# Kernel optimization log

Hardware: AMD Instinct MI355X
Metric: run time of the kernel (lower is better)

## Reference

```python
import jax, jax.numpy as jnp
from jax import lax
import numpy as np

B, H, W = 2048, 28, 28
LATENT_EACH = 64
LATENT = 2 * LATENT_EACH  # 128
MEM_SIZE = 8192
TOPK = 10
EPS = 1e-12


def _conv(x, w, b):
    # x: NCHW, w: OIHW, 3x3 conv, padding=1 (SAME)
    y = lax.conv_general_dilated(x, w, (1, 1), 'SAME',
                                 dimension_numbers=('NCHW', 'OIHW', 'NCHW'))
    return y + b[None, :, None, None]


def _deconv(x, w, b):
    # ConvTranspose2d(k=4, stride=2, padding=1) -> out = 2*in (SAME transpose)
    # w: HWIO = (4,4,in,out)
    y = lax.conv_transpose(x, w, (2, 2), 'SAME',
                           dimension_numbers=('NCHW', 'HWIO', 'NCHW'))
    return y + b[None, :, None, None]


def _encoder(x, w1, b1, w2, b2, fcw, fcb):
    h = jax.nn.relu(_conv(x, w1, b1))
    h = jax.nn.relu(_conv(h, w2, b2))
    feat = h.mean(axis=(2, 3))  # AdaptiveAvgPool2d((1,1)) + flatten -> [B,64]
    return feat @ fcw.T + fcb


def _memory_match(z, mem):
    mn = mem / jnp.maximum(jnp.linalg.norm(mem, axis=1, keepdims=True), EPS)
    zn = z / jnp.maximum(jnp.linalg.norm(z, axis=1, keepdims=True), EPS)
    sim = zn @ mn.T                      # [B, MEM_SIZE]
    topv, topi = lax.top_k(sim, TOPK)    # [B, K]
    wts = jax.nn.softmax(topv, axis=1)   # [B, K]
    sel = mem[topi]                      # gather: [B, K, LATENT]
    return jnp.einsum('bk,bkd->bd', wts, sel)


def setup_inputs() -> dict:
    key = jax.random.key(0)
    ks = jax.random.split(key, 24)
    g = lambda k, s, scale=0.05: jax.random.normal(k, s, jnp.float32) * scale
    inp = {
        'x': jax.random.normal(ks[0], (B, 1, H, W), jnp.float32),
        # center encoder
        'ce_w1': g(ks[1], (32, 1, 3, 3)), 'ce_b1': jnp.zeros((32,), jnp.float32),
        'ce_w2': g(ks[2], (64, 32, 3, 3)), 'ce_b2': jnp.zeros((64,), jnp.float32),
        'ce_fcw': g(ks[3], (LATENT_EACH, 64)), 'ce_fcb': jnp.zeros((LATENT_EACH,), jnp.float32),
        # global encoder
        'ge_w1': g(ks[4], (32, 1, 3, 3)), 'ge_b1': jnp.zeros((32,), jnp.float32),
        'ge_w2': g(ks[5], (64, 32, 3, 3)), 'ge_b2': jnp.zeros((64,), jnp.float32),
        'ge_fcw': g(ks[6], (LATENT_EACH, 64)), 'ge_fcb': jnp.zeros((LATENT_EACH,), jnp.float32),
        # memory bank (Parameter ~ randn)
        'mem': jax.random.normal(ks[7], (MEM_SIZE, LATENT), jnp.float32),
        # decoder
        'dec_fcw': g(ks[8], (64 * 7 * 7, LATENT)), 'dec_fcb': jnp.zeros((64 * 7 * 7,), jnp.float32),
        'd_w1': g(ks[9], (4, 4, 64, 32)), 'd_b1': jnp.zeros((32,), jnp.float32),   # deconv 64->32
        'd_w2': g(ks[10], (16, 32, 3, 3)), 'd_b2': jnp.zeros((16,), jnp.float32),  # conv 32->16
        'd_w3': g(ks[11], (4, 4, 16, 8)), 'd_b3': jnp.zeros((8,), jnp.float32),    # deconv 16->8
        'd_w4': g(ks[12], (1, 8, 3, 3)), 'd_b4': jnp.zeros((1,), jnp.float32),     # conv 8->1
    }
    return inp


def reference(x, ce_w1, ce_b1, ce_w2, ce_b2, ce_fcw, ce_fcb,
              ge_w1, ge_b1, ge_w2, ge_b2, ge_fcw, ge_fcb,
              mem, dec_fcw, dec_fcb,
              d_w1, d_b1, d_w2, d_b2, d_w3, d_b3, d_w4, d_b4):
    # crop_center(x, 14): start = (28-14)//2 = 7
    x_center = x[:, :, 7:21, 7:21]
    z_center = _encoder(x_center, ce_w1, ce_b1, ce_w2, ce_b2, ce_fcw, ce_fcb)
    z_global = _encoder(x, ge_w1, ge_b1, ge_w2, ge_b2, ge_fcw, ge_fcb)
    z = jnp.concatenate([z_center, z_global], axis=1)  # [B, 128]
    z_match = _memory_match(z, mem)                    # [B, 128]
    d = (z_match @ dec_fcw.T + dec_fcb).reshape(B, 64, 7, 7)
    d = jax.nn.relu(_deconv(d, d_w1, d_b1))   # [B,32,14,14]
    d = jax.nn.relu(_conv(d, d_w2, d_b2))     # [B,16,14,14]
    d = jax.nn.relu(_deconv(d, d_w3, d_b3))   # [B,8,28,28]
    x_hat = _conv(d, d_w4, d_b4)              # [B,1,28,28]
    return x_hat
```

## Files before the change

### kernel.cpp

```cpp
#include <hip/hip_runtime.h>
#include <cfloat>
#include <cmath>

#define TPB 256

typedef _Float16 half8 __attribute__((ext_vector_type(8)));
typedef float floatx16 __attribute__((ext_vector_type(16)));
typedef float floatx4 __attribute__((ext_vector_type(4)));

__device__ __forceinline__ float wave_reduce_sum(float v) {
#pragma unroll
  for (int off = 32; off > 0; off >>= 1) v += __shfl_xor(v, off, 64);
  return v;
}

__global__ __launch_bounds__(64) void prep_bfrags(
    const float* __restrict__ ce_w2, const float* __restrict__ ge_w2,
    float* __restrict__ frags) {
  const int blk = blockIdx.x;
  const int enc = blk / 72;
  const int frag = blk % 72;
  const int ks = frag >> 2, part = (frag >> 1) & 1, nt = frag & 1;
  const int tap = ks >> 1, half = ks & 1;
  const int lane = threadIdx.x;
  const float* w2 = enc ? ge_w2 : ce_w2;
  const int n = nt * 32 + (lane & 31);
  const int cb = half * 16 + (lane >> 5) * 8;
  half8 out;
#pragma unroll
  for (int j = 0; j < 8; ++j) {
    float v = w2[(n * 32 + cb + j) * 9 + tap];
    _Float16 h = (_Float16)v;
    out[j] = (part == 0) ? h : (_Float16)((v - (float)h) * 4096.f);
  }
  *(half8*)((char*)frags + ((size_t)blk * 64 + lane) * 16) = out;
}

__global__ __launch_bounds__(64) void prep_dec1(
    const float* __restrict__ w1, float* __restrict__ frags) {
  const int blk = blockIdx.x;
  const int phase = blk >> 4, ks = blk & 15;
  const int pa = phase >> 1, pb = phase & 1;
  const int st = ks >> 2, kk = ks & 3;
  const int s = st >> 1, tt = st & 1;
  const int lane = threadIdx.x;
  const int kg = lane >> 5, n = lane & 31;
  const int tap = (pa + 2 * s) * 4 + (pb + 2 * tt);
  half8 o;
#pragma unroll
  for (int j = 0; j < 8; ++j) {
    int c = kk * 16 + kg * 8 + j;
    o[j] = (_Float16)w1[tap * 2048 + c * 32 + n];
  }
  *(half8*)((char*)frags + ((size_t)blk * 64 + lane) * 16) = o;
}

__global__ __launch_bounds__(64) void prep_dfc(
    const float* __restrict__ dfcw, float* __restrict__ frags) {
  const int blk = blockIdx.x;
  const int nt = blk >> 3, ks = blk & 7;
  const int lane = threadIdx.x;
  const int n = lane & 31, kg = lane >> 5;
  const int j = nt * 32 + n;
  const int px = j >> 6, c = j & 63;
  half8 o;
#pragma unroll
  for (int u = 0; u < 8; ++u)
    o[u] = (_Float16)dfcw[(size_t)(c * 49 + px) * 128 + ks * 16 + kg * 8 + u];
  *(half8*)((char*)frags + ((size_t)blk * 64 + lane) * 16) = o;
}

__global__ __launch_bounds__(256) void norm_kernel(
    const float* __restrict__ memg, float* __restrict__ invn) {
  const int wv = threadIdx.x >> 6, lane = threadIdx.x & 63;
  const int row = blockIdx.x * 4 + wv;
  const float* r = memg + (size_t)row * 128;
  float a = r[lane], b = r[lane + 64];
  float s = wave_reduce_sum(a * a + b * b);
  if (lane == 0) invn[row] = 1.f / fmaxf(sqrtf(s), 1e-12f);
}

template <int S, bool CENTER>
__device__ __forceinline__ void encoder_body(
    char* smem, const float* __restrict__ x, const float* __restrict__ w1,
    const float* __restrict__ b1, const float* __restrict__ b2,
    const float* __restrict__ fcw, const float* __restrict__ fcb,
    const float* __restrict__ bfrag, float* __restrict__ zout, int zoff,
    int b) {
  constexpr int SP = S + 2;
  constexpr int NBANDS = (S == 28) ? 3 : 2;
  constexpr int RMAX = 12;
  constexpr int NPIX = RMAX * SP;
  constexpr int GSTB = NPIX * 16;
  constexpr int PSTB = 4 * GSTB;

  char* h1s = smem;
  float* xs = (float*)(smem + 2 * PSTB);
  float* w1s = xs + SP * SP;
  float(*featp)[64] = (float(*)[64])(w1s + 288);

  const int t = threadIdx.x;
  const int lane = t & 63;
  const int wv = t >> 6;

  for (int e = t; e < SP * SP; e += TPB) xs[e] = 0.f;
  for (int e = t; e < 288; e += TPB) w1s[e] = w1[e];
  __syncthreads();
  const float* xb = x + (size_t)b * 784 + (CENTER ? (7 * 28 + 7) : 0);
  for (int e = t; e < S * S; e += TPB) {
    int i = e / S, j = e - i * S;
    xs[(i + 1) * SP + (j + 1)] = xb[i * 28 + j];
  }

  float sp0 = 0.f, sp1 = 0.f;
  const float bias0 = b2[lane & 31];
  const float bias1 = b2[32 + (lane & 31)];
  const int gOff = (lane >> 5) * GSTB;
  const char* bgbase = (const char*)bfrag + lane * 16;

#pragma unroll
  for (int band = 0; band < NBANDS; ++band) {
    const int BH_ = (S == 28) ? ((band < 2) ? 10 : 8) : ((band == 0) ? 10 : 4);
    const int b0 = band * 10;
    const int LIMIT = BH_ * S;
    const int MTB = (LIMIT + 31) / 32;
    const int NBLK2 = (MTB + 1) / 2;

    __syncthreads();
    for (int e = t; e < 4 * NPIX; e += TPB) {
      int g = e / NPIX;
      int pix = e - g * NPIX;
      int lr = pix / SP;
      int cw = pix - lr * SP;
      int gr = b0 - 1 + lr;
      int ebase = g * GSTB + pix * 16;
      half8 hi8 = {}, lo8 = {};
      if (gr >= 0 && gr < S && cw >= 1 && cw <= S) {
        float xv[9];
#pragma unroll
        for (int di = 0; di < 3; ++di)
#pragma unroll
          for (int dj = 0; dj < 3; ++dj)
            xv[di * 3 + dj] = xs[(gr + di) * SP + (cw - 1 + dj)];
#pragma unroll
        for (int u = 0; u < 8; ++u) {
          int ch = g * 8 + u;
          float a = b1[ch];
#pragma unroll
          for (int v = 0; v < 9; ++v) a += xv[v] * w1s[ch * 9 + v];
          a = fmaxf(a, 0.f);
          _Float16 h = (_Float16)a;
          hi8[u] = h;
          lo8[u] = (_Float16)((a - (float)h) * 4096.f);
        }
      }
      *(half8*)(h1s + ebase) = hi8;
      *(half8*)(h1s + PSTB + ebase) = lo8;
    }
    __syncthreads();
    for (int mblk = wv; mblk < NBLK2; mblk += 4) {
      const int Mt0 = mblk * 2;
      floatx16 acc[2][2][2] = {};
      int pixB[2];
#pragma unroll
      for (int im = 0; im < 2; ++im) {
        int px = (Mt0 + im) * 32 + (lane & 31);
        px = px < LIMIT ? px : LIMIT - 1;
        int r = px / S;
        int cc = px - r * S;
        pixB[im] = (r * SP + cc) * 16;
      }
#pragma unroll 3
      for (int tap = 0; tap < 9; ++tap) {
        const int di = tap / 3, dj = tap - di * 3;
        const int offT = (di * SP + dj) * 16;
#pragma unroll
        for (int half = 0; half < 2; ++half) {
          const int ks = tap * 2 + half;
          const char* bp = bgbase + ks * 4096;
          const int offA = offT + gOff + half * (2 * GSTB);
          half8 ah0 = *(const half8*)(h1s + pixB[0] + offA);
          half8 al0 = *(const half8*)(h1s + PSTB + pixB[0] + offA);
          half8 ah1 = *(const half8*)(h1s + pixB[1] + offA);
          half8 al1 = *(const half8*)(h1s + PSTB + pixB[1] + offA);
          {
            half8 bh = *(const half8*)(bp);
            half8 bl = *(const half8*)(bp + 2048);
            acc[0][0][0] = __builtin_amdgcn_mfma_f32_32x32x16_f16(
                ah0, bh, acc[0][0][0], 0, 0, 0);
            acc[0][0][1] = __builtin_amdgcn_mfma_f32_32x32x16_f16(
                ah0, bl, acc[0][0][1], 0, 0, 0);
            acc[0][0][1] = __builtin_amdgcn_mfma_f32_32x32x16_f16(
                al0, bh, acc[0][0][1], 0, 0, 0);
            acc[1][0][0] = __builtin_amdgcn_mfma_f32_32x32x16_f16(
                ah1, bh, acc[1][0][0], 0, 0, 0);
            acc[1][0][1] = __builtin_amdgcn_mfma_f32_32x32x16_f16(
                ah1, bl, acc[1][0][1], 0, 0, 0);
            acc[1][0][1] = __builtin_amdgcn_mfma_f32_32x32x16_f16(
                al1, bh, acc[1][0][1], 0, 0, 0);
          }
          {
            half8 bh = *(const half8*)(bp + 1024);
            half8 bl = *(const half8*)(bp + 3072);
            acc[0][1][0] = __builtin_amdgcn_mfma_f32_32x32x16_f16(
                ah0, bh, acc[0][1][0], 0, 0, 0);
            acc[0][1][1] = __builtin_amdgcn_mfma_f32_32x32x16_f16(
                ah0, bl, acc[0][1][1], 0, 0, 0);
            acc[0][1][1] = __builtin_amdgcn_mfma_f32_32x32x16_f16(
                al0, bh, acc[0][1][1], 0, 0, 0);
            acc[1][1][0] = __builtin_amdgcn_mfma_f32_32x32x16_f16(
                ah1, bh, acc[1][1][0], 0, 0, 0);
            acc[1][1][1] = __builtin_amdgcn_mfma_f32_32x32x16_f16(
                ah1, bl, acc[1][1][1], 0, 0, 0);
            acc[1][1][1] = __builtin_amdgcn_mfma_f32_32x32x16_f16(
                al1, bh, acc[1][1][1], 0, 0, 0);
          }
        }
      }
#pragma unroll
      for (int im = 0; im < 2; ++im)
#pragma unroll
        for (int reg = 0; reg < 16; ++reg) {
          int row = (reg & 3) + 8 * (reg >> 2) + 4 * (lane >> 5);
          int p = (Mt0 + im) * 32 + row;
          if (p < LIMIT) {
            float v0 =
                acc[im][0][0][reg] + acc[im][0][1][reg] * (1.f / 4096.f) + bias0;
            float v1 =
                acc[im][1][0][reg] + acc[im][1][1][reg] * (1.f / 4096.f) + bias1;
            sp0 += fmaxf(v0, 0.f);
            sp1 += fmaxf(v1, 0.f);
          }
        }
    }
  }
  sp0 += __shfl_xor(sp0, 32);
  sp1 += __shfl_xor(sp1, 32);
  if (lane < 32) {
    featp[wv][lane] = sp0;
    featp[wv][32 + lane] = sp1;
  }
  __syncthreads();
  if (t < 64)
    featp[0][t] = (featp[0][t] + featp[1][t] + featp[2][t] + featp[3][t]) *
                  (1.f / (S * S));
  __syncthreads();
  if (t < 64) {
    float s = 0.f;
#pragma unroll
    for (int i = 0; i < 64; ++i) s += featp[0][i] * fcw[t * 64 + i];
    zout[(size_t)b * 128 + zoff + t] = s + fcb[t];
  }
}

__global__ __launch_bounds__(256, 3) void encoders_fused(
    const float* __restrict__ x, const float* __restrict__ ce_w1,
    const float* __restrict__ ce_b1, const float* __restrict__ ce_b2,
    const float* __restrict__ ce_fcw, const float* __restrict__ ce_fcb,
    const float* __restrict__ ge_w1, const float* __restrict__ ge_b1,
    const float* __restrict__ ge_b2, const float* __restrict__ ge_fcw,
    const float* __restrict__ ge_fcb, const float* __restrict__ frags,
    float* __restrict__ z) {
  __shared__ __align__(16) char smem[51856];
  if (blockIdx.x < 2048)
    encoder_body<28, false>(smem, x, ge_w1, ge_b1, ge_b2, ge_fcw, ge_fcb,
                            frags + 18432, z, 64, blockIdx.x);
  else
    encoder_body<14, true>(smem, x, ce_w1, ce_b1, ce_b2, ce_fcw, ce_fcb, frags,
                           z, 0, blockIdx.x - 2048);
}

__global__ __launch_bounds__(256) void match_part(
    const float* __restrict__ z, const float* __restrict__ memg,
    const float* __restrict__ invn, float* __restrict__ topvw,
    int* __restrict__ topiw) {
  __shared__ __align__(16) float zs[8][128];
  __shared__ float qv[8][512];
  __shared__ int qi[8][512];
  __shared__ int qn[8];
  __shared__ float rowmin[8];

  const int t = threadIdx.x;
  const int rowbase = blockIdx.x * 8;
  const int mbase = blockIdx.y * 2048;

  for (int e = t; e < 8 * 128; e += TPB) {
    int r = e >> 7, j = e & 127;
    zs[r][j] = z[(size_t)(rowbase + r) * 128 + j];
  }
  if (t < 8) { qn[t] = 0; rowmin[t] = -FLT_MAX; }
  __syncthreads();
  {
    int wv = t >> 6, lane = t & 63;
#pragma unroll
    for (int h = 0; h < 2; ++h) {
      int r = wv + h * 4;
      float a = zs[r][lane], b = zs[r][lane + 64];
      float s = wave_reduce_sum(a * a + b * b);
      float inv = 1.f / fmaxf(sqrtf(s), 1e-12f);
      zs[r][lane] = a * inv;
      zs[r][lane + 64] = b * inv;
    }
  }
  __syncthreads();

  float av[10];
  int ai[10];
#pragma unroll
  for (int i = 0; i < 10; ++i) { av[i] = -FLT_MAX; ai[i] = 0; }

  for (int mt = 0; mt < 4; ++mt) {
    int m0 = mbase + mt * 512 + t;
    float acc0[8] = {}, acc1[8] = {};
    const float4* mr0 = (const float4*)(memg + (size_t)m0 * 128);
    const float4* mr1 = (const float4*)(memg + (size_t)(m0 + 256) * 128);
#pragma unroll 4
    for (int jq = 0; jq < 32; ++jq) {
      float4 a0 = mr0[jq], a1 = mr1[jq];
#pragma unroll
      for (int r = 0; r < 8; ++r) {
        float4 zv = ((const float4*)zs[r])[jq];
        acc0[r] += a0.x * zv.x + a0.y * zv.y + a0.z * zv.z + a0.w * zv.w;
        acc1[r] += a1.x * zv.x + a1.y * zv.y + a1.z * zv.z + a1.w * zv.w;
      }
    }
    float i0 = invn[m0], i1 = invn[m0 + 256];
#pragma unroll
    for (int r = 0; r < 8; ++r) {
      float rm = rowmin[r];
      float v0 = acc0[r] * i0;
      if (v0 > rm) {
        int k = atomicAdd(&qn[r], 1);
        qv[r][k] = v0; qi[r][k] = m0;
      }
      float v1 = acc1[r] * i1;
      if (v1 > rm) {
        int k = atomicAdd(&qn[r], 1);
        qv[r][k] = v1; qi[r][k] = m0 + 256;
      }
    }
    __syncthreads();
    if (t < 8) {
      int n = qn[t];
      for (int k = 0; k < n; ++k) {
        float v = qv[t][k];
        int m = qi[t][k];
        if (v > av[9]) {
#pragma unroll
          for (int i = 0; i < 10; ++i) {
            if (v > av[i]) {
              float tv = av[i]; av[i] = v; v = tv;
              int ti = ai[i]; ai[i] = m; m = ti;
            }
          }
        }
      }
      qn[t] = 0;
      rowmin[t] = av[9];
    }
    __syncthreads();
  }

  if (t < 8) {
    const size_t base = (size_t)(rowbase + t) * 40 + blockIdx.y * 10;
#pragma unroll
    for (int k = 0; k < 10; ++k) {
      topvw[base + k] = av[k];
      topiw[base + k] = ai[k];
    }
  }
}

__global__ __launch_bounds__(256) void match_merge(
    const float* __restrict__ topvw, const int* __restrict__ topiw,
    const float* __restrict__ memg, _Float16* __restrict__ zmf16) {
  __shared__ float topw[8][10];
  __shared__ int topidx[8][10];
  const int t = threadIdx.x;
  const int rowbase = blockIdx.x * 8;

  if (t < 8) {
    float av[10];
    int ai[10];
#pragma unroll
    for (int i = 0; i < 10; ++i) { av[i] = -FLT_MAX; ai[i] = 0; }
    const size_t base = (size_t)(rowbase + t) * 40;
    for (int c = 0; c < 40; ++c) {
      float v = topvw[base + c];
      int m = topiw[base + c];
      if (v > av[9]) {
#pragma unroll
        for (int i = 0; i < 10; ++i) {
          if (v > av[i]) {
            float tv = av[i]; av[i] = v; v = tv;
            int ti = ai[i]; ai[i] = m; m = ti;
          }
        }
      }
    }
    float e_[10], s = 0.f;
#pragma unroll
    for (int k = 0; k < 10; ++k) { e_[k] = expf(av[k]); s += e_[k]; }
    float inv = 1.f / s;
#pragma unroll
    for (int k = 0; k < 10; ++k) { topw[t][k] = e_[k] * inv; topidx[t][k] = ai[k]; }
  }
  __syncthreads();
  for (int e = t; e < 8 * 128; e += TPB) {
    int r = e >> 7, d = e & 127;
    float o = 0.f;
#pragma unroll
    for (int k = 0; k < 10; ++k)
      o += topw[r][k] * memg[(size_t)topidx[r][k] * 128 + d];
    zmf16[(size_t)(rowbase + r) * 128 + d] = (_Float16)o;
  }
}

__global__ __launch_bounds__(256) void decfc_kernel(
    const _Float16* __restrict__ zmf16, const float* __restrict__ fcb,
    const float* __restrict__ dfcfrags, _Float16* __restrict__ d0f16) {
  const int t = threadIdx.x;
  const int lane = t & 63;
  const int wv = t >> 6;
  const int r0 = blockIdx.x * 32;
  const int ntbase = blockIdx.y * 49;

  half8 a[8];
  {
    const _Float16* ap =
        zmf16 + (size_t)(r0 + (lane & 31)) * 128 + (lane >> 5) * 8;
#pragma unroll
    for (int ks = 0; ks < 8; ++ks) a[ks] = *(const half8*)(ap + ks * 16);
  }
  const char* fb = (const char*)dfcfrags + lane * 16;

  for (int nt = ntbase + wv; nt < ntbase + 49; nt += 4) {
    half8 bfr[8];
    const char* p = fb + (size_t)nt * 8192;
#pragma unroll
    for (int ks = 0; ks < 8; ++ks) bfr[ks] = *(const half8*)(p + ks * 1024);
    floatx16 acc = {};
#pragma unroll
    for (int ks = 0; ks < 8; ++ks)
      acc = __builtin_amdgcn_mfma_f32_32x32x16_f16(a[ks], bfr[ks], acc, 0, 0, 0);
    const int col = nt * 32 + (lane & 31);
    const int px = col >> 6, c = col & 63;
    const float bias = fcb[c * 49 + px];
#pragma unroll
    for (int reg = 0; reg < 16; ++reg) {
      int row = (reg & 3) + 8 * (reg >> 2) + 4 * (lane >> 5);
      d0f16[((size_t)(r0 + row) * 49 + px) * 64 + c] = (_Float16)(acc[reg] + bias);
    }
  }
}

__global__ __launch_bounds__(256) void decoder_kernel(
    const _Float16* __restrict__ d0f16, const float* __restrict__ b1,
    const float* __restrict__ w2, const float* __restrict__ b2,
    const float* __restrict__ w3, const float* __restrict__ b3,
    const float* __restrict__ w4, const float* __restrict__ b4,
    const float* __restrict__ dec1frags, float* __restrict__ out) {
  __shared__ __align__(16) char dsm[41408];
  char* d0f = dsm;
  float* d2 = (float*)dsm;
  char* d1f = dsm + 12608;
  char* w2s = dsm + 28992;
  float* d3 = (float*)(dsm + 12608);

  const int b = blockIdx.x;
  const int t = threadIdx.x;
  const int lane = t & 63;
  const int wv = t >> 6;

  for (int e = t; e < 648; e += TPB) {
    int g = e / 81, pix = e - g * 81;
    int ih = pix / 9 - 1, iw = pix % 9 - 1;
    half8 hv = {};
    if (ih >= 0 && ih < 7 && iw >= 0 && iw < 7)
      hv = *(const half8*)(d0f16 + ((size_t)b * 49 + ih * 7 + iw) * 64 + g * 8);
    *(half8*)(d0f + e * 16) = hv;
  }
  for (int e = t; e < 576; e += TPB) {
    int tau = e / 64, l = e - tau * 64;
    int n = l & 15, kq = l >> 4;
    half8 v;
#pragma unroll
    for (int u = 0; u < 8; ++u)
      v[u] = (_Float16)w2[(n * 32 + kq * 8 + u) * 9 + tau];
    *(half8*)(w2s + e * 16) = v;
  }
  for (int e = t; e < 1024; e += TPB)
    *(float4*)(d1f + e * 16) = make_float4(0.f, 0.f, 0.f, 0.f);
  __syncthreads();

  {
    const int pa = wv >> 1, pb = wv & 1;
    const int kg = lane >> 5, o = lane & 31;
    const char* bg = (const char*)dec1frags + wv * 16384 + lane * 16;
    int pxa[2][4];
#pragma unroll
    for (int im = 0; im < 2; ++im) {
      int px = im * 32 + o;
      px = px < 49 ? px : 48;
      int i = px / 7, j2 = px - i * 7;
#pragma unroll
      for (int st = 0; st < 4; ++st) {
        int s = st >> 1, tt = st & 1;
        pxa[im][st] = ((i + pa + s) * 9 + (j2 + pb + tt)) * 16;
      }
    }
    floatx16 acc0 = {}, acc1 = {};
    half8 nb = *(const half8*)(bg);
#pragma unroll
    for (int ks = 0; ks < 16; ++ks) {
      half8 bf = nb;
      if (ks < 15) nb = *(const half8*)(bg + (ks + 1) * 1024);
      const int gbase = (((ks & 3) * 2 + kg) * 81) * 16;
      half8 a0 = *(const half8*)(d0f + gbase + pxa[0][ks >> 2]);
      half8 a1 = *(const half8*)(d0f + gbase + pxa[1][ks >> 2]);
      acc0 = __builtin_amdgcn_mfma_f32_32x32x16_f16(a0, bf, acc0, 0, 0, 0);
      acc1 = __builtin_amdgcn_mfma_f32_32x32x16_f16(a1, bf, acc1, 0, 0, 0);
    }
    const float bias = b1[o];
    char* dst = d1f + (o >> 3) * 4096 + (o & 7) * 2;
#pragma unroll
    for (int im = 0; im < 2; ++im) {
      const floatx16& ac = im ? acc1 : acc0;
#pragma unroll
      for (int reg = 0; reg < 16; ++reg) {
        int row = (reg & 3) + 8 * (reg >> 2) + 4 * kg;
        int px = im * 32 + row;
        if (px < 49) {
          int i = px / 7, j2 = px - i * 7;
          int p = 2 * i + pa, q = 2 * j2 + pb;
          *(_Float16*)(dst + ((p + 1) * 16 + (q + 1)) * 16) =
              (_Float16)fmaxf(ac[reg] + bias, 0.f);
        }
      }
    }
  }
  __syncthreads();

  {
    const int m = lane & 15, kq = lane >> 4;
    half8 bq[9];
#pragma unroll
    for (int tau = 0; tau < 9; ++tau)
      bq[tau] = *(const half8*)(w2s + (tau * 64 + lane) * 16);
    for (int mt = wv; mt < 13; mt += 4) {
      int px = mt * 16 + m;
      px = px < 196 ? px : 195;
      const int p = px / 14, q = px - (px / 14) * 14;
      floatx4 acc = {};
#pragma unroll
      for (int tau = 0; tau < 9; ++tau) {
        const int dp = tau / 3, dq = tau - dp * 3;
        half8 av =
            *(const half8*)(d1f + (kq * 256 + (p + dp) * 16 + (q + dq)) * 16);
        acc = __builtin_amdgcn_mfma_f32_16x16x32_f16(av, bq[tau], acc, 0, 0, 0);
      }
      const int o = lane & 15;
      const float bias = b2[o];
#pragma unroll
      for (int reg = 0; reg < 4; ++reg) {
        int row = (lane >> 4) * 4 + reg;
        int opx = mt * 16 + row;
        if (opx < 196) d2[o * 197 + opx] = fmaxf(acc[reg] + bias, 0.f);
      }
    }
  }
  __syncthreads();
  for (int e = t; e < 7200; e += TPB) d3[e] = 0.f;
  __syncthreads();

  {
    const int ph = __builtin_amdgcn_readfirstlane(t >> 6);
    const int pa = ph >> 1, pb = ph & 1;
    const int tb = pa * 4 + pb;
    const float* wA = w3 + (size_t)tb * 128;
    const float* wB = w3 + (size_t)(tb + 2) * 128;
    const float* wC = w3 + (size_t)(tb + 8) * 128;
    const float* wD = w3 + (size_t)(tb + 10) * 128;
#pragma unroll 1
    for (int k = 0; k < 4; ++k) {
      const int px = lane + 64 * k;
      const int cpx = px < 196 ? px : 195;
      const int i = cpx / 14, j = cpx % 14;
      int ih[2], iw[2];
      float mh[2], mw[2];
#pragma unroll
      for (int s = 0; s < 2; ++s) {
        int v = i + pa + s - 1;
        mh[s] = (v >= 0 && v <= 13) ? 1.f : 0.f;
        ih[s] = v < 0 ? 0 : (v > 13 ? 13 : v);
        int u = j + pb + s - 1;
        mw[s] = (u >= 0 && u <= 13) ? 1.f : 0.f;
        iw[s] = u < 0 ? 0 : (u > 13 ? 13 : u);
      }
      const float m00 = mh[0] * mw[0], m01 = mh[0] * mw[1];
      const float m10 = mh[1] * mw[0], m11 = mh[1] * mw[1];
      float acc[8];
#pragma unroll
      for (int oo = 0; oo < 8; ++oo) acc[oo] = b3[oo];
#pragma unroll 2
      for (int c = 0; c < 16; ++c) {
        const float a00 = d2[c * 197 + ih[0] * 14 + iw[0]] * m00;
        const float a01 = d2[c * 197 + ih[0] * 14 + iw[1]] * m01;
        const float a10 = d2[c * 197 + ih[1] * 14 + iw[0]] * m10;
        const float a11 = d2[c * 197 + ih[1] * 14 + iw[1]] * m11;
        const int wb = c * 8;
#pragma unroll
        for (int oo = 0; oo < 8; ++oo)
          acc[oo] += a00 * wA[wb + oo] + a01 * wB[wb + oo] +
                     a10 * wC[wb + oo] + a11 * wD[wb + oo];
      }
      if (px < 196) {
        const int p = 2 * i + pa, q = 2 * j + pb;
        const int widx = (p + 1) * 30 + (q + 1);
#pragma unroll
        for (int oo = 0; oo < 8; ++oo)
          d3[oo * 900 + widx] = fmaxf(acc[oo], 0.f);
      }
    }
  }
  __syncthreads();

  for (int e = t; e < 784; e += TPB) {
    int p = e / 28, q = e - p * 28;
    float a = b4[0];
#pragma unroll
    for (int c = 0; c < 8; ++c) {
      const float* bp = &d3[c * 900 + p * 30 + q];
#pragma unroll
      for (int di = 0; di < 3; ++di)
#pragma unroll
        for (int dj = 0; dj < 3; ++dj)
          a += bp[di * 30 + dj] * w4[c * 9 + di * 3 + dj];
    }
    out[(size_t)b * 784 + e] = a;
  }
}

extern "C" void kernel_launch(void* const* d_in, const int* in_sizes, int n_in,
                              void* d_out, int out_size, void* d_ws,
                              size_t ws_size, hipStream_t stream) {
  const float* x      = (const float*)d_in[0];
  const float* ce_w1  = (const float*)d_in[1];
  const float* ce_b1  = (const float*)d_in[2];
  const float* ce_w2  = (const float*)d_in[3];
  const float* ce_b2  = (const float*)d_in[4];
  const float* ce_fcw = (const float*)d_in[5];
  const float* ce_fcb = (const float*)d_in[6];
  const float* ge_w1  = (const float*)d_in[7];
  const float* ge_b1  = (const float*)d_in[8];
  const float* ge_w2  = (const float*)d_in[9];
  const float* ge_b2  = (const float*)d_in[10];
  const float* ge_fcw = (const float*)d_in[11];
  const float* ge_fcb = (const float*)d_in[12];
  const float* memg   = (const float*)d_in[13];
  const float* dfcw   = (const float*)d_in[14];
  const float* dfcb   = (const float*)d_in[15];
  const float* d_w1   = (const float*)d_in[16];
  const float* d_b1   = (const float*)d_in[17];
  const float* d_w2   = (const float*)d_in[18];
  const float* d_b2   = (const float*)d_in[19];
  const float* d_w3   = (const float*)d_in[20];
  const float* d_b3   = (const float*)d_in[21];
  const float* d_w4   = (const float*)d_in[22];
  const float* d_b4   = (const float*)d_in[23];
  float* outp = (float*)d_out;

  float*     ws        = (float*)d_ws;
  float*     z         = ws;
  _Float16*  zmf16     = (_Float16*)(ws + 262144);
  float*     invn      = ws + 262144 + 131072;
  float*     frags     = invn + 8192;
  float*     dec1frags = frags + 36864;
  float*     dfcfrags  = dec1frags + 16384;
  float*     tailbase  = dfcfrags + 200704;
  float*     topvw     = tailbase;
  int*       topiw     = (int*)(tailbase + 81920);
  _Float16*  d0f16     = (_Float16*)tailbase;

  prep_bfrags<<<144, 64, 0, stream>>>(ce_w2, ge_w2, frags);
  prep_dec1<<<64, 64, 0, stream>>>(d_w1, dec1frags);
  prep_dfc<<<784, 64, 0, stream>>>(dfcw, dfcfrags);
  norm_kernel<<<2048, TPB, 0, stream>>>(memg, invn);
  encoders_fused<<<4096, TPB, 0, stream>>>(x, ce_w1, ce_b1, ce_b2, ce_fcw,
                                           ce_fcb, ge_w1, ge_b1, ge_b2, ge_fcw,
                                           ge_fcb, frags, z);
  match_part<<<dim3(256, 4), TPB, 0, stream>>>(z, memg, invn, topvw, topiw);
  match_merge<<<256, TPB, 0, stream>>>(topvw, topiw, memg, zmf16);
  decfc_kernel<<<dim3(64, 2), TPB, 0, stream>>>(zmf16, dfcb, dfcfrags, d0f16);
  decoder_kernel<<<2048, TPB, 0, stream>>>(d0f16, d_b1, d_w2, d_b2, d_w3, d_b3,
                                           d_w4, d_b4, dec1frags, outp);
}
```

Measured before the change: 711.7 us.

## Compute memory similarity with split-fp16 MFMA instead of scalar FP32 dot products

The similarity matmul between normalized latents and the memory bank now runs on 32x32x16 fp16 MFMA instructions. Both operands are split into high and scaled low fp16 parts, and three MFMAs per k-step recover near-fp32 accuracy. A new prep kernel converts the memory bank into fragment layout in each call. The match kernel tiles 32 rows by 16 column groups, so the merge stage now reduces 160 candidates per row instead of 40. This trades extra prep traffic and a larger merge for much higher matmul throughput, at some risk to top-k ordering from reduced precision.

```diff
diff --git a/kernel.cpp b/kernel.cpp
--- a/kernel.cpp
+++ b/kernel.cpp
@@ -67,6 +67,25 @@
 #pragma unroll
   for (int u = 0; u < 8; ++u)
     o[u] = (_Float16)dfcw[(size_t)(c * 49 + px) * 128 + ks * 16 + kg * 8 + u];
+  *(half8*)((char*)frags + ((size_t)blk * 64 + lane) * 16) = o;
+}
+
+__global__ __launch_bounds__(64) void prep_mem(
+    const float* __restrict__ memg, float* __restrict__ frags) {
+  const int blk = blockIdx.x;
+  const int slot = blk & 15;
+  const int p = slot >> 3, ks = slot & 7;
+  const int T = blk >> 4;
+  const int lane = threadIdx.x;
+  const int n = lane & 31, kg = lane >> 5;
+  const float* src = memg + (size_t)(T * 32 + n) * 128 + ks * 16 + kg * 8;
+  half8 o;
+#pragma unroll
+  for (int j = 0; j < 8; ++j) {
+    float v = src[j];
+    _Float16 h = (_Float16)v;
+    o[j] = p ? (_Float16)((v - (float)h) * 4096.f) : h;
+  }
   *(half8*)((char*)frags + ((size_t)blk * 64 + lane) * 16) = o;
 }
 
@@ -270,87 +289,101 @@
                            z, 0, blockIdx.x - 2048);
 }
 
-__global__ __launch_bounds__(256) void match_part(
-    const float* __restrict__ z, const float* __restrict__ memg,
+__global__ __launch_bounds__(256) void match_mfma(
+    const float* __restrict__ z, const float* __restrict__ memfrags,
     const float* __restrict__ invn, float* __restrict__ topvw,
     int* __restrict__ topiw) {
-  __shared__ __align__(16) float zs[8][128];
-  __shared__ float qv[8][512];
-  __shared__ int qi[8][512];
-  __shared__ int qn[8];
-  __shared__ float rowmin[8];
+  __shared__ __align__(16) char smem[49408];
+  float* zs = (float*)smem;
+  float* qv = (float*)smem;
+  int* qi = (int*)(smem + 16384);
+  char* zfrag = smem + 32768;
+  float* rowmin = (float*)(smem + 49152);
+  int* qn = (int*)(smem + 49152 + 128);
 
   const int t = threadIdx.x;
-  const int rowbase = blockIdx.x * 8;
-  const int mbase = blockIdx.y * 2048;
-
-  for (int e = t; e < 8 * 128; e += TPB) {
-    int r = e >> 7, j = e & 127;
-    zs[r][j] = z[(size_t)(rowbase + r) * 128 + j];
-  }
-  if (t < 8) { qn[t] = 0; rowmin[t] = -FLT_MAX; }
-  __syncthreads();
+  const int lane = t & 63;
+  const int wv = t >> 6;
+  const int rowbase = blockIdx.x * 32;
+  const int Tbase = blockIdx.y * 16;
+
+  for (int e = t; e < 4096; e += TPB) zs[e] = z[(size_t)rowbase * 128 + e];
+  if (t < 32) { rowmin[t] = -FLT_MAX; qn[t] = 0; }
+  __syncthreads();
+#pragma unroll
+  for (int h = 0; h < 8; ++h) {
+    int r = wv * 8 + h;
+    float a = zs[r * 128 + lane], b = zs[r * 128 + 64 + lane];
+    float s = wave_reduce_sum(a * a + b * b);
+    float inv = 1.f / fmaxf(sqrtf(s), 1e-12f);
+    zs[r * 128 + lane] = a * inv;
+    zs[r * 128 + 64 + lane] = b * inv;
+  }
+  __syncthreads();
+  for (int e = t; e < 4096; e += TPB) {
+    int m = e >> 7, c = e & 127;
+    float v = zs[m * 128 + c];
+    _Float16 h = (_Float16)v;
+    _Float16 l = (_Float16)((v - (float)h) * 4096.f);
+    int ks = c >> 4, kg = (c >> 3) & 1, j = c & 7;
+    int off = (ks * 64 + kg * 32 + m) * 16 + j * 2;
+    *(_Float16*)(zfrag + off) = h;
+    *(_Float16*)(zfrag + 8192 + off) = l;
+  }
+  __syncthreads();
+
+  half8 ah[8], al[8];
   {
-    int wv = t >> 6, lane = t & 63;
-#pragma unroll
-    for (int h = 0; h < 2; ++h) {
-      int r = wv + h * 4;
-      float a = zs[r][lane], b = zs[r][lane + 64];
-      float s = wave_reduce_sum(a * a + b * b);
-      float inv = 1.f / fmaxf(sqrtf(s), 1e-12f);
-      zs[r][lane] = a * inv;
-      zs[r][lane + 64] = b * inv;
-    }
-  }
-  __syncthreads();
+    const char* zf = zfrag + ((lane >> 5) * 32 + (lane & 31)) * 16;
+#pragma unroll
+    for (int ks = 0; ks < 8; ++ks) {
+      ah[ks] = *(const half8*)(zf + ks * 1024);
+      al[ks] = *(const half8*)(zf + 8192 + ks * 1024);
+    }
+  }
 
   float av[10];
   int ai[10];
 #pragma unroll
   for (int i = 0; i < 10; ++i) { av[i] = -FLT_MAX; ai[i] = 0; }
 
-  for (int mt = 0; mt < 4; ++mt) {
-    int m0 = mbase + mt * 512 + t;
-    float acc0[8] = {}, acc1[8] = {};
-    const float4* mr0 = (const float4*)(memg + (size_t)m0 * 128);
-    const float4* mr1 = (const float4*)(memg + (size_t)(m0 + 256) * 128);
-#pragma unroll 4
-    for (int jq = 0; jq < 32; ++jq) {
-      float4 a0 = mr0[jq], a1 = mr1[jq];
-#pragma unroll
-      for (int r = 0; r < 8; ++r) {
-        float4 zv = ((const float4*)zs[r])[jq];
-        acc0[r] += a0.x * zv.x + a0.y * zv.y + a0.z * zv.z + a0.w * zv.w;
-        acc1[r] += a1.x * zv.x + a1.y * zv.y + a1.z * zv.z + a1.w * zv.w;
-      }
-    }
-    float i0 = invn[m0], i1 = invn[m0 + 256];
-#pragma unroll
-    for (int r = 0; r < 8; ++r) {
-      float rm = rowmin[r];
-      float v0 = acc0[r] * i0;
-      if (v0 > rm) {
-        int k = atomicAdd(&qn[r], 1);
-        qv[r][k] = v0; qi[r][k] = m0;
-      }
-      float v1 = acc1[r] * i1;
-      if (v1 > rm) {
-        int k = atomicAdd(&qn[r], 1);
-        qv[r][k] = v1; qi[r][k] = m0 + 256;
+#pragma unroll 1
+  for (int round = 0; round < 4; ++round) {
+    const int T = Tbase + round * 4 + wv;
+    const char* bf = (const char*)memfrags + (size_t)T * 16384 + lane * 16;
+    floatx16 acc0 = {}, acc1 = {};
+#pragma unroll
+    for (int ks = 0; ks < 8; ++ks) {
+      half8 bh = *(const half8*)(bf + ks * 1024);
+      half8 bl = *(const half8*)(bf + 8192 + ks * 1024);
+      acc0 = __builtin_amdgcn_mfma_f32_32x32x16_f16(ah[ks], bh, acc0, 0, 0, 0);
+      acc1 = __builtin_amdgcn_mfma_f32_32x32x16_f16(ah[ks], bl, acc1, 0, 0, 0);
+      acc1 = __builtin_amdgcn_mfma_f32_32x32x16_f16(al[ks], bh, acc1, 0, 0, 0);
+    }
+    const int gn = T * 32 + (lane & 31);
+    const float iv = invn[gn];
+#pragma unroll
+    for (int reg = 0; reg < 16; ++reg) {
+      int m = (reg & 3) + 8 * (reg >> 2) + 4 * (lane >> 5);
+      float v = (acc0[reg] + acc1[reg] * (1.f / 4096.f)) * iv;
+      if (v > rowmin[m]) {
+        int k = atomicAdd(&qn[m], 1);
+        qv[m * 128 + k] = v;
+        qi[m * 128 + k] = gn;
       }
     }
     __syncthreads();
-    if (t < 8) {
+    if (t < 32) {
       int n = qn[t];
       for (int k = 0; k < n; ++k) {
-        float v = qv[t][k];
-        int m = qi[t][k];
+        float v = qv[t * 128 + k];
+        int mm = qi[t * 128 + k];
         if (v > av[9]) {
 #pragma unroll
           for (int i = 0; i < 10; ++i) {
             if (v > av[i]) {
               float tv = av[i]; av[i] = v; v = tv;
-              int ti = ai[i]; ai[i] = m; m = ti;
+              int ti = ai[i]; ai[i] = mm; mm = ti;
             }
           }
         }
@@ -361,8 +394,8 @@
     __syncthreads();
   }
 
-  if (t < 8) {
-    const size_t base = (size_t)(rowbase + t) * 40 + blockIdx.y * 10;
+  if (t < 32) {
+    const size_t base = (size_t)(rowbase + t) * 160 + blockIdx.y * 10;
 #pragma unroll
     for (int k = 0; k < 10; ++k) {
       topvw[base + k] = av[k];
@@ -384,8 +417,8 @@
     int ai[10];
 #pragma unroll
     for (int i = 0; i < 10; ++i) { av[i] = -FLT_MAX; ai[i] = 0; }
-    const size_t base = (size_t)(rowbase + t) * 40;
-    for (int c = 0; c < 40; ++c) {
+    const size_t base = (size_t)(rowbase + t) * 160;
+    for (int c = 0; c < 160; ++c) {
       float v = topvw[base + c];
       int m = topiw[base + c];
       if (v > av[9]) {
@@ -677,19 +710,21 @@
   float*     frags     = invn + 8192;
   float*     dec1frags = frags + 36864;
   float*     dfcfrags  = dec1frags + 16384;
-  float*     tailbase  = dfcfrags + 200704;
+  float*     memfrags  = dfcfrags + 200704;
+  float*     tailbase  = memfrags + 1048576;
   float*     topvw     = tailbase;
-  int*       topiw     = (int*)(tailbase + 81920);
+  int*       topiw     = (int*)(tailbase + 327680);
   _Float16*  d0f16     = (_Float16*)tailbase;
 
   prep_bfrags<<<144, 64, 0, stream>>>(ce_w2, ge_w2, frags);
   prep_dec1<<<64, 64, 0, stream>>>(d_w1, dec1frags);
   prep_dfc<<<784, 64, 0, stream>>>(dfcw, dfcfrags);
+  prep_mem<<<4096, 64, 0, stream>>>(memg, memfrags);
   norm_kernel<<<2048, TPB, 0, stream>>>(memg, invn);
   encoders_fused<<<4096, TPB, 0, stream>>>(x, ce_w1, ce_b1, ce_b2, ce_fcw,
                                            ce_fcb, ge_w1, ge_b1, ge_b2, ge_fcw,
                                            ge_fcb, frags, z);
-  match_part<<<dim3(256, 4), TPB, 0, stream>>>(z, memg, invn, topvw, topiw);
+  match_mfma<<<dim3(64, 16), TPB, 0, stream>>>(z, memfrags, invn, topvw, topiw);
   match_merge<<<256, TPB, 0, stream>>>(topvw, topiw, memg, zmf16);
   decfc_kernel<<<dim3(64, 2), TPB, 0, stream>>>(zmf16, dfcb, dfcfrags, d0f16);
   decoder_kernel<<<2048, TPB, 0, stream>>>(d0f16, d_b1, d_w2, d_b2, d_w3, d_b3,
```

Measured after the change: 681.9 us. 4.2% less time.
